# Kernel optimization log

Hardware: AMD Instinct MI355X
Metric: run time of the kernel (lower is better)

Reference implementation:

```python
import jax, jax.numpy as jnp
import numpy as np

H = 256  # hidden_dim
B = 256  # batch
T = 512  # seq_len


def setup_inputs() -> dict:
    key = jax.random.key(0)
    ks = jax.random.split(key, 16)
    s_in = 1.0  # torch LSTMCell init: U(-1/sqrt(H), 1/sqrt(H)); use scaled normal for simplicity
    sc = 1.0 / np.sqrt(H)
    inp = {
        "input": jax.random.normal(ks[0], (B, T), dtype=jnp.float32),
        # layer 1: input_size = 1
        "W_ih1": jax.random.uniform(ks[1], (4 * H, 1), jnp.float32, -sc, sc),
        "W_hh1": jax.random.uniform(ks[2], (4 * H, H), jnp.float32, -sc, sc),
        "b_ih1": jax.random.uniform(ks[3], (4 * H,), jnp.float32, -sc, sc),
        "b_hh1": jax.random.uniform(ks[4], (4 * H,), jnp.float32, -sc, sc),
        # layer 2
        "W_ih2": jax.random.uniform(ks[5], (4 * H, H), jnp.float32, -sc, sc),
        "W_hh2": jax.random.uniform(ks[6], (4 * H, H), jnp.float32, -sc, sc),
        "b_ih2": jax.random.uniform(ks[7], (4 * H,), jnp.float32, -sc, sc),
        "b_hh2": jax.random.uniform(ks[8], (4 * H,), jnp.float32, -sc, sc),
        # layer 3
        "W_ih3": jax.random.uniform(ks[9], (4 * H, H), jnp.float32, -sc, sc),
        "W_hh3": jax.random.uniform(ks[10], (4 * H, H), jnp.float32, -sc, sc),
        "b_ih3": jax.random.uniform(ks[11], (4 * H,), jnp.float32, -sc, sc),
        "b_hh3": jax.random.uniform(ks[12], (4 * H,), jnp.float32, -sc, sc),
        # output head Linear(H, 1)
        "W_lin": jax.random.uniform(ks[13], (1, H), jnp.float32, -sc, sc),
        "b_lin": jax.random.uniform(ks[14], (1,), jnp.float32, -sc, sc),
    }
    return inp


def _lstm_cell(x, h, c, Wi, Wh, bi, bh):
    # PyTorch LSTMCell gate order: i, f, g, o
    gates = x @ Wi.T + bi + h @ Wh.T + bh  # [B, 4H]
    i, f, g, o = jnp.split(gates, 4, axis=-1)
    c_new = jax.nn.sigmoid(f) * c + jax.nn.sigmoid(i) * jnp.tanh(g)
    h_new = jax.nn.sigmoid(o) * jnp.tanh(c_new)
    return h_new, c_new


def reference(input, W_ih1, W_hh1, b_ih1, b_hh1, W_ih2, W_hh2, b_ih2, b_hh2,
              W_ih3, W_hh3, b_ih3, b_hh3, W_lin, b_lin):
    n = input.shape[0]
    z = jnp.zeros((n, H), dtype=jnp.float32)
    init = (z, z, z, z, z, z)  # (h1, c1, h2, c2, h3, c3)
    xs = input.T[:, :, None]  # [T, B, 1]

    def step(carry, x_t):
        h1, c1, h2, c2, h3, c3 = carry
        h1, c1 = _lstm_cell(x_t, h1, c1, W_ih1, W_hh1, b_ih1, b_hh1)
        h2, c2 = _lstm_cell(h1, h2, c2, W_ih2, W_hh2, b_ih2, b_hh2)
        h3, c3 = _lstm_cell(h2, h3, c3, W_ih3, W_hh3, b_ih3, b_hh3)
        y = h3 @ W_lin.T + b_lin  # [B, 1] (dropout p=0 is identity)
        return (h1, c1, h2, c2, h3, c3), y

    _, ys = jax.lax.scan(step, init, xs)  # ys: [T, B, 1]
    return ys[:, :, 0].T  # [B, T], matches torch.cat(outputs, dim=1)
```

## Files before the change

kernel.cpp:

```cpp
#include <hip/hip_runtime.h>
#include <stdint.h>


#define Hd 256
#define Bd 256
#define Td 512
#define RING 4
#define GH 8
#define GB 8
#define CPAD 32

typedef __attribute__((ext_vector_type(8))) short short8;
typedef __attribute__((ext_vector_type(4))) float floatx4;
typedef __attribute__((ext_vector_type(4))) unsigned int uintx4;

__device__ __forceinline__ unsigned short f2bf(float f) {
  union { float f; unsigned int u; } v; v.f = f;
  return (unsigned short)((v.u + 0x7fffu + ((v.u >> 16) & 1u)) >> 16);
}
__device__ __forceinline__ float sigm(float x) { return 1.0f / (1.0f + __expf(-x)); }
__device__ __forceinline__ float tanhfast(float x) { return 2.0f / (1.0f + __expf(-2.0f * x)) - 1.0f; }

__device__ __forceinline__ void spin_relaxed(unsigned int* p, unsigned int v) {
  while (__hip_atomic_load(p, __ATOMIC_RELAXED, __HIP_MEMORY_SCOPE_AGENT) < v) { }
}

__global__ __launch_bounds__(512, 2) void lstm3_kernel(
    const float* __restrict__ xin,
    const float* __restrict__ Wi1, const float* __restrict__ Wh1,
    const float* __restrict__ bi1, const float* __restrict__ bh1,
    const float* __restrict__ Wi2, const float* __restrict__ Wh2,
    const float* __restrict__ bi2, const float* __restrict__ bh2,
    const float* __restrict__ Wi3, const float* __restrict__ Wh3,
    const float* __restrict__ bi3, const float* __restrict__ bh3,
    const float* __restrict__ Wlin, const float* __restrict__ blin,
    float* __restrict__ out,
    unsigned int* __restrict__ cnt,
    unsigned short* __restrict__ ring)
{
  __shared__ float gl[4][32][33];
  __shared__ uintx4 hbuf[2][1024];

  const int bid = blockIdx.x;
  const int j   = bid / 24;
  const int rem = bid - j * 24;
  const int l   = rem >> 3;
  const int g   = rem & 7;

  const int tid  = threadIdx.x;
  const int lane = tid & 63;
  const int wave = tid >> 6;
  const int tau  = wave & 3;
  const int mh   = wave >> 2;
  const int quad = lane >> 4;
  const int l15  = lane & 15;

  const int ubase = j * 32;
  const int rbase = g * 32;

  const float* Wpi = (l == 1) ? Wi2 : Wi3;
  const float* Wph = (l == 0) ? Wh1 : ((l == 1) ? Wh2 : Wh3);
  const float* bi  = (l == 0) ? bi1 : ((l == 1) ? bi2 : bi3);
  const float* bh  = (l == 0) ? bh1 : ((l == 1) ? bh2 : bh3);

  short8 breg[2][16];
  {
    const int koff = quad * 8;
    #pragma unroll
    for (int nt = 0; nt < 2; ++nt) {
      const int grow = tau * Hd + ubase + nt * 16 + l15;
      #pragma unroll
      for (int kc = 0; kc < 16; ++kc) {
        short8 v = {0, 0, 0, 0, 0, 0, 0, 0};
        const float* src = nullptr;
        if (kc < 8) { if (l != 0) src = Wpi + (size_t)grow * Hd + kc * 32 + koff; }
        else        { src = Wph + (size_t)grow * Hd + (kc - 8) * 32 + koff; }
        if (src) {
          #pragma unroll
          for (int e = 0; e < 8; ++e) v[e] = (short)f2bf(src[e]);
        }
        breg[nt][kc] = v;
      }
    }
  }

  const int clrow = tid >> 4;
  const int cu0   = (tid & 15) * 2;
  float bsum[4][2], wiv[4][2], wlv[2];
  #pragma unroll
  for (int tt = 0; tt < 4; ++tt) {
    #pragma unroll
    for (int du = 0; du < 2; ++du) {
      const int gg = tt * Hd + ubase + cu0 + du;
      bsum[tt][du] = bi[gg] + bh[gg];
      wiv[tt][du]  = (l == 0) ? Wi1[gg] : 0.0f;
    }
  }
  wlv[0] = (l == 2) ? Wlin[ubase + cu0]     : 0.0f;
  wlv[1] = (l == 2) ? Wlin[ubase + cu0 + 1] : 0.0f;
  const float bl0 = (l == 2 && j == 0) ? blin[0] : 0.0f;

  float cst0 = 0.0f, cst1 = 0.0f;

  unsigned int* myC = cnt + (l * GB + g) * CPAD;
  unsigned int* upC = cnt + ((l - 1) * GB + g) * CPAD;
  unsigned int* dnC = cnt + ((l + 1) * GB + g) * CPAD;
  unsigned short* ownR = ring + (size_t)l * RING * Bd * Hd;
  const unsigned short* upRb = ring + (size_t)(l - 1) * RING * Bd * Hd;

  const float* xrow = xin + (size_t)(rbase + clrow) * Td;

  const int c0 = tid;
  const int c1 = tid + 512;
  const int o0 = ((c0 >> 2) & 31) * 512 + (c0 >> 7) * 64 + (c0 & 3) * 16;
  const int o1 = ((c1 >> 2) & 31) * 512 + (c1 >> 7) * 64 + (c1 & 3) * 16;
  const int fragbase = (mh * 16 + l15) * 4 + quad;

  {
    uintx4 z = {0u, 0u, 0u, 0u};
    hbuf[1][c0] = z;
    hbuf[1][c1] = z;
  }

  for (int t = 0; t < Td; ++t) {
    {
      bool active = false; unsigned int* p = nullptr; unsigned need = 0;
      if (tid == 0)      { active = (t > 0);                p = myC; need = GH * t; }
      else if (tid == 1) { active = (l > 0);                p = upC; need = GH * (t + 1); }
      else if (tid == 2) { active = (l < 2) && (t >= RING); p = dnC; need = GH * (t - RING + 1); }
      if (active) spin_relaxed(p, need);
    }
    __syncthreads();

    uintx4 u0, u1, v0, v1;
    if (l != 0) {
      const char* upReg = (const char*)(upRb + (size_t)(t & (RING - 1)) * Bd * Hd
                                        + (size_t)rbase * Hd);
      asm volatile("global_load_dwordx4 %0, %1, off sc0 sc1"
                   : "=&v"(u0) : "v"(upReg + o0));
      asm volatile("global_load_dwordx4 %0, %1, off sc0 sc1"
                   : "=&v"(u1) : "v"(upReg + o1));
    }
    if (t != 0) {
      const char* ownReg = (const char*)(ownR + (size_t)((t + RING - 1) & (RING - 1)) * Bd * Hd
                                         + (size_t)rbase * Hd);
      asm volatile("global_load_dwordx4 %0, %1, off sc0 sc1"
                   : "=&v"(v0) : "v"(ownReg + o0));
      asm volatile("global_load_dwordx4 %0, %1, off sc0 sc1"
                   : "=&v"(v1) : "v"(ownReg + o1));
    }
    asm volatile("s_waitcnt vmcnt(0)" ::: "memory");
    if (l != 0) { hbuf[0][c0] = u0; hbuf[0][c1] = u1; }
    if (t != 0) { hbuf[1][c0] = v0; hbuf[1][c1] = v1; }
    __syncthreads();

    short8 av[16];
    if (l != 0) {
      #pragma unroll
      for (int kc = 0; kc < 8; ++kc)
        av[kc] = *reinterpret_cast<const short8*>(&hbuf[0][kc * 128 + fragbase]);
    }
    #pragma unroll
    for (int kc = 0; kc < 8; ++kc)
      av[8 + kc] = *reinterpret_cast<const short8*>(&hbuf[1][kc * 128 + fragbase]);

    floatx4 acc0 = {0.f, 0.f, 0.f, 0.f};
    floatx4 acc1 = {0.f, 0.f, 0.f, 0.f};
    if (l != 0) {
      #pragma unroll
      for (int kc = 0; kc < 8; ++kc) {
        acc0 = __builtin_amdgcn_mfma_f32_16x16x32_bf16(av[kc], breg[0][kc], acc0, 0, 0, 0);
        acc1 = __builtin_amdgcn_mfma_f32_16x16x32_bf16(av[kc], breg[1][kc], acc1, 0, 0, 0);
      }
    }
    #pragma unroll
    for (int kc = 8; kc < 16; ++kc) {
      acc0 = __builtin_amdgcn_mfma_f32_16x16x32_bf16(av[kc], breg[0][kc], acc0, 0, 0, 0);
      acc1 = __builtin_amdgcn_mfma_f32_16x16x32_bf16(av[kc], breg[1][kc], acc1, 0, 0, 0);
    }

    {
      const int lr = mh * 16 + quad * 4;
      #pragma unroll
      for (int r2 = 0; r2 < 4; ++r2) {
        gl[tau][lr + r2][l15]      = acc0[r2];
        gl[tau][lr + r2][16 + l15] = acc1[r2];
      }
    }
    __syncthreads();

    float h0, h1;
    {
      const float xv = (l == 0) ? xrow[t] : 0.0f;
      float pi = gl[0][clrow][cu0] + bsum[0][0] + xv * wiv[0][0];
      float pf = gl[1][clrow][cu0] + bsum[1][0] + xv * wiv[1][0];
      float pg = gl[2][clrow][cu0] + bsum[2][0] + xv * wiv[2][0];
      float po = gl[3][clrow][cu0] + bsum[3][0] + xv * wiv[3][0];
      float ii = sigm(pi), ff = sigm(pf), gv = tanhfast(pg), oo = sigm(po);
      cst0 = ff * cst0 + ii * gv;
      h0 = oo * tanhfast(cst0);
      pi = gl[0][clrow][cu0 + 1] + bsum[0][1] + xv * wiv[0][1];
      pf = gl[1][clrow][cu0 + 1] + bsum[1][1] + xv * wiv[1][1];
      pg = gl[2][clrow][cu0 + 1] + bsum[2][1] + xv * wiv[2][1];
      po = gl[3][clrow][cu0 + 1] + bsum[3][1] + xv * wiv[3][1];
      ii = sigm(pi); ff = sigm(pf); gv = tanhfast(pg); oo = sigm(po);
      cst1 = ff * cst1 + ii * gv;
      h1 = oo * tanhfast(cst1);
    }

    {
      unsigned short* dst = ownR + (size_t)(t & (RING - 1)) * Bd * Hd
                          + (size_t)(rbase + clrow) * Hd + ubase + cu0;
      const unsigned int packed = (unsigned int)f2bf(h0) | ((unsigned int)f2bf(h1) << 16);
      __hip_atomic_store((unsigned int*)dst, packed, __ATOMIC_RELAXED,
                         __HIP_MEMORY_SCOPE_AGENT);
    }

    if (l == 2) {
      float pr = wlv[0] * h0 + wlv[1] * h1;
      pr += __shfl_xor(pr, 8);
      pr += __shfl_xor(pr, 4);
      pr += __shfl_xor(pr, 2);
      pr += __shfl_xor(pr, 1);
      if ((tid & 15) == 0) {
        atomicAdd(&out[(size_t)(rbase + clrow) * Td + t], pr + bl0);
      }
    }

    __syncthreads();
    if (tid == 0) {
      __hip_atomic_fetch_add(myC, 1u, __ATOMIC_RELAXED, __HIP_MEMORY_SCOPE_AGENT);
    }
  }
}

extern "C" void kernel_launch(void* const* d_in, const int* in_sizes, int n_in,
                              void* d_out, int out_size, void* d_ws, size_t ws_size,
                              hipStream_t stream) {
  const float* xin  = (const float*)d_in[0];
  const float* Wi1  = (const float*)d_in[1];
  const float* Wh1  = (const float*)d_in[2];
  const float* bi1  = (const float*)d_in[3];
  const float* bh1  = (const float*)d_in[4];
  const float* Wi2  = (const float*)d_in[5];
  const float* Wh2  = (const float*)d_in[6];
  const float* bi2  = (const float*)d_in[7];
  const float* bh2  = (const float*)d_in[8];
  const float* Wi3  = (const float*)d_in[9];
  const float* Wh3  = (const float*)d_in[10];
  const float* bi3  = (const float*)d_in[11];
  const float* bh3  = (const float*)d_in[12];
  const float* Wlin = (const float*)d_in[13];
  const float* blin = (const float*)d_in[14];
  float* out = (float*)d_out;

  unsigned int*   cnt  = (unsigned int*)d_ws;
  unsigned short* ring = (unsigned short*)((char*)d_ws + 4096);

  hipMemsetAsync(d_ws, 0, 4096, stream);
  hipMemsetAsync(d_out, 0, (size_t)out_size * sizeof(float), stream);

  lstm3_kernel<<<dim3(3 * GB * GH), dim3(512), 0, stream>>>(
      xin, Wi1, Wh1, bi1, bh1, Wi2, Wh2, bi2, bh2,
      Wi3, Wh3, bi3, bh3, Wlin, blin, out, cnt, ring);
}
```

Measured before the change: 1.663 ms.

## Double threads per block to split gate columns across more waves

Raises the block size from 512 to 1024 threads so each wave computes one 16-column MFMA tile instead of two, halving per-wave weight registers and per-thread loads and cell updates. The h-state store now packs neighbouring units through a lane shuffle, and the output reduction covers 32 lanes. This shortens each thread's serial work per timestep, since the recurrence is latency bound, but allows only one block per CU and adds more waves to every barrier.

```diff
diff --git a/kernel.cpp b/kernel.cpp
--- a/kernel.cpp
+++ b/kernel.cpp
@@ -25,7 +25,7 @@
   while (__hip_atomic_load(p, __ATOMIC_RELAXED, __HIP_MEMORY_SCOPE_AGENT) < v) { }
 }
 
-__global__ __launch_bounds__(512, 2) void lstm3_kernel(
+__global__ __launch_bounds__(1024, 1) void lstm3_kernel(
     const float* __restrict__ xin,
     const float* __restrict__ Wi1, const float* __restrict__ Wh1,
     const float* __restrict__ bi1, const float* __restrict__ bh1,
@@ -51,7 +51,8 @@
   const int lane = tid & 63;
   const int wave = tid >> 6;
   const int tau  = wave & 3;
-  const int mh   = wave >> 2;
+  const int mh   = (wave >> 2) & 1;
+  const int ub   = wave >> 3;
   const int quad = lane >> 4;
   const int l15  = lane & 15;
 
@@ -63,44 +64,37 @@
   const float* bi  = (l == 0) ? bi1 : ((l == 1) ? bi2 : bi3);
   const float* bh  = (l == 0) ? bh1 : ((l == 1) ? bh2 : bh3);
 
-  short8 breg[2][16];
+  short8 breg[16];
   {
     const int koff = quad * 8;
+    const int grow = tau * Hd + ubase + ub * 16 + l15;
     #pragma unroll
-    for (int nt = 0; nt < 2; ++nt) {
-      const int grow = tau * Hd + ubase + nt * 16 + l15;
-      #pragma unroll
-      for (int kc = 0; kc < 16; ++kc) {
-        short8 v = {0, 0, 0, 0, 0, 0, 0, 0};
-        const float* src = nullptr;
-        if (kc < 8) { if (l != 0) src = Wpi + (size_t)grow * Hd + kc * 32 + koff; }
-        else        { src = Wph + (size_t)grow * Hd + (kc - 8) * 32 + koff; }
-        if (src) {
-          #pragma unroll
-          for (int e = 0; e < 8; ++e) v[e] = (short)f2bf(src[e]);
-        }
-        breg[nt][kc] = v;
-      }
-    }
-  }
-
-  const int clrow = tid >> 4;
-  const int cu0   = (tid & 15) * 2;
-  float bsum[4][2], wiv[4][2], wlv[2];
+    for (int kc = 0; kc < 16; ++kc) {
+      short8 v = {0, 0, 0, 0, 0, 0, 0, 0};
+      const float* src = nullptr;
+      if (kc < 8) { if (l != 0) src = Wpi + (size_t)grow * Hd + kc * 32 + koff; }
+      else        { src = Wph + (size_t)grow * Hd + (kc - 8) * 32 + koff; }
+      if (src) {
+        #pragma unroll
+        for (int e = 0; e < 8; ++e) v[e] = (short)f2bf(src[e]);
+      }
+      breg[kc] = v;
+    }
+  }
+
+  const int clrow = tid >> 5;
+  const int cu    = tid & 31;
+  float bsum[4], wiv[4];
   #pragma unroll
   for (int tt = 0; tt < 4; ++tt) {
-    #pragma unroll
-    for (int du = 0; du < 2; ++du) {
-      const int gg = tt * Hd + ubase + cu0 + du;
-      bsum[tt][du] = bi[gg] + bh[gg];
-      wiv[tt][du]  = (l == 0) ? Wi1[gg] : 0.0f;
-    }
-  }
-  wlv[0] = (l == 2) ? Wlin[ubase + cu0]     : 0.0f;
-  wlv[1] = (l == 2) ? Wlin[ubase + cu0 + 1] : 0.0f;
+    const int gg = tt * Hd + ubase + cu;
+    bsum[tt] = bi[gg] + bh[gg];
+    wiv[tt]  = (l == 0) ? Wi1[gg] : 0.0f;
+  }
+  const float wlv = (l == 2) ? Wlin[ubase + cu] : 0.0f;
   const float bl0 = (l == 2 && j == 0) ? blin[0] : 0.0f;
 
-  float cst0 = 0.0f, cst1 = 0.0f;
+  float cst = 0.0f;
 
   unsigned int* myC = cnt + (l * GB + g) * CPAD;
   unsigned int* upC = cnt + ((l - 1) * GB + g) * CPAD;
@@ -111,15 +105,12 @@
   const float* xrow = xin + (size_t)(rbase + clrow) * Td;
 
   const int c0 = tid;
-  const int c1 = tid + 512;
-  const int o0 = ((c0 >> 2) & 31) * 512 + (c0 >> 7) * 64 + (c0 & 3) * 16;
-  const int o1 = ((c1 >> 2) & 31) * 512 + (c1 >> 7) * 64 + (c1 & 3) * 16;
+  const int o0 = ((tid >> 2) & 31) * 512 + (tid >> 7) * 64 + (tid & 3) * 16;
   const int fragbase = (mh * 16 + l15) * 4 + quad;
 
   {
     uintx4 z = {0u, 0u, 0u, 0u};
     hbuf[1][c0] = z;
-    hbuf[1][c1] = z;
   }
 
   for (int t = 0; t < Td; ++t) {
@@ -132,97 +123,78 @@
     }
     __syncthreads();
 
-    uintx4 u0, u1, v0, v1;
+    uintx4 u0, v0;
     if (l != 0) {
       const char* upReg = (const char*)(upRb + (size_t)(t & (RING - 1)) * Bd * Hd
                                         + (size_t)rbase * Hd);
       asm volatile("global_load_dwordx4 %0, %1, off sc0 sc1"
                    : "=&v"(u0) : "v"(upReg + o0));
-      asm volatile("global_load_dwordx4 %0, %1, off sc0 sc1"
-                   : "=&v"(u1) : "v"(upReg + o1));
     }
     if (t != 0) {
       const char* ownReg = (const char*)(ownR + (size_t)((t + RING - 1) & (RING - 1)) * Bd * Hd
                                          + (size_t)rbase * Hd);
       asm volatile("global_load_dwordx4 %0, %1, off sc0 sc1"
                    : "=&v"(v0) : "v"(ownReg + o0));
-      asm volatile("global_load_dwordx4 %0, %1, off sc0 sc1"
-                   : "=&v"(v1) : "v"(ownReg + o1));
     }
     asm volatile("s_waitcnt vmcnt(0)" ::: "memory");
-    if (l != 0) { hbuf[0][c0] = u0; hbuf[0][c1] = u1; }
-    if (t != 0) { hbuf[1][c0] = v0; hbuf[1][c1] = v1; }
-    __syncthreads();
-
-    short8 av[16];
-    if (l != 0) {
-      #pragma unroll
-      for (int kc = 0; kc < 8; ++kc)
-        av[kc] = *reinterpret_cast<const short8*>(&hbuf[0][kc * 128 + fragbase]);
-    }
-    #pragma unroll
-    for (int kc = 0; kc < 8; ++kc)
-      av[8 + kc] = *reinterpret_cast<const short8*>(&hbuf[1][kc * 128 + fragbase]);
-
-    floatx4 acc0 = {0.f, 0.f, 0.f, 0.f};
-    floatx4 acc1 = {0.f, 0.f, 0.f, 0.f};
+    if (l != 0) { hbuf[0][c0] = u0; }
+    if (t != 0) { hbuf[1][c0] = v0; }
+    __syncthreads();
+
+    floatx4 acc = {0.f, 0.f, 0.f, 0.f};
     if (l != 0) {
       #pragma unroll
       for (int kc = 0; kc < 8; ++kc) {
-        acc0 = __builtin_amdgcn_mfma_f32_16x16x32_bf16(av[kc], breg[0][kc], acc0, 0, 0, 0);
-        acc1 = __builtin_amdgcn_mfma_f32_16x16x32_bf16(av[kc], breg[1][kc], acc1, 0, 0, 0);
+        const short8 av = *reinterpret_cast<const short8*>(&hbuf[0][kc * 128 + fragbase]);
+        acc = __builtin_amdgcn_mfma_f32_16x16x32_bf16(av, breg[kc], acc, 0, 0, 0);
       }
     }
     #pragma unroll
     for (int kc = 8; kc < 16; ++kc) {
-      acc0 = __builtin_amdgcn_mfma_f32_16x16x32_bf16(av[kc], breg[0][kc], acc0, 0, 0, 0);
-      acc1 = __builtin_amdgcn_mfma_f32_16x16x32_bf16(av[kc], breg[1][kc], acc1, 0, 0, 0);
+      const short8 av = *reinterpret_cast<const short8*>(&hbuf[1][(kc - 8) * 128 + fragbase]);
+      acc = __builtin_amdgcn_mfma_f32_16x16x32_bf16(av, breg[kc], acc, 0, 0, 0);
     }
 
     {
       const int lr = mh * 16 + quad * 4;
       #pragma unroll
       for (int r2 = 0; r2 < 4; ++r2) {
-        gl[tau][lr + r2][l15]      = acc0[r2];
-        gl[tau][lr + r2][16 + l15] = acc1[r2];
-      }
-    }
-    __syncthreads();
-
-    float h0, h1;
+        gl[tau][lr + r2][ub * 16 + l15] = acc[r2];
+      }
+    }
+    __syncthreads();
+
+    float h0;
     {
       const float xv = (l == 0) ? xrow[t] : 0.0f;
-      float pi = gl[0][clrow][cu0] + bsum[0][0] + xv * wiv[0][0];
-      float pf = gl[1][clrow][cu0] + bsum[1][0] + xv * wiv[1][0];
-      float pg = gl[2][clrow][cu0] + bsum[2][0] + xv * wiv[2][0];
-      float po = gl[3][clrow][cu0] + bsum[3][0] + xv * wiv[3][0];
-      float ii = sigm(pi), ff = sigm(pf), gv = tanhfast(pg), oo = sigm(po);
-      cst0 = ff * cst0 + ii * gv;
-      h0 = oo * tanhfast(cst0);
-      pi = gl[0][clrow][cu0 + 1] + bsum[0][1] + xv * wiv[0][1];
-      pf = gl[1][clrow][cu0 + 1] + bsum[1][1] + xv * wiv[1][1];
-      pg = gl[2][clrow][cu0 + 1] + bsum[2][1] + xv * wiv[2][1];
-      po = gl[3][clrow][cu0 + 1] + bsum[3][1] + xv * wiv[3][1];
-      ii = sigm(pi); ff = sigm(pf); gv = tanhfast(pg); oo = sigm(po);
-      cst1 = ff * cst1 + ii * gv;
-      h1 = oo * tanhfast(cst1);
-    }
-
-    {
-      unsigned short* dst = ownR + (size_t)(t & (RING - 1)) * Bd * Hd
-                          + (size_t)(rbase + clrow) * Hd + ubase + cu0;
-      const unsigned int packed = (unsigned int)f2bf(h0) | ((unsigned int)f2bf(h1) << 16);
-      __hip_atomic_store((unsigned int*)dst, packed, __ATOMIC_RELAXED,
-                         __HIP_MEMORY_SCOPE_AGENT);
+      const float pi = gl[0][clrow][cu] + bsum[0] + xv * wiv[0];
+      const float pf = gl[1][clrow][cu] + bsum[1] + xv * wiv[1];
+      const float pg = gl[2][clrow][cu] + bsum[2] + xv * wiv[2];
+      const float po = gl[3][clrow][cu] + bsum[3] + xv * wiv[3];
+      const float ii = sigm(pi), ff = sigm(pf), gv = tanhfast(pg), oo = sigm(po);
+      cst = ff * cst + ii * gv;
+      h0 = oo * tanhfast(cst);
+    }
+
+    {
+      const float hn = __shfl_xor(h0, 1);
+      if ((cu & 1) == 0) {
+        unsigned short* dst = ownR + (size_t)(t & (RING - 1)) * Bd * Hd
+                            + (size_t)(rbase + clrow) * Hd + ubase + cu;
+        const unsigned int packed = (unsigned int)f2bf(h0) | ((unsigned int)f2bf(hn) << 16);
+        __hip_atomic_store((unsigned int*)dst, packed, __ATOMIC_RELAXED,
+                           __HIP_MEMORY_SCOPE_AGENT);
+      }
     }
 
     if (l == 2) {
-      float pr = wlv[0] * h0 + wlv[1] * h1;
+      float pr = wlv * h0;
+      pr += __shfl_xor(pr, 16);
       pr += __shfl_xor(pr, 8);
       pr += __shfl_xor(pr, 4);
       pr += __shfl_xor(pr, 2);
       pr += __shfl_xor(pr, 1);
-      if ((tid & 15) == 0) {
+      if ((tid & 31) == 0) {
         atomicAdd(&out[(size_t)(rbase + clrow) * Td + t], pr + bl0);
       }
     }
@@ -260,7 +232,7 @@
   hipMemsetAsync(d_ws, 0, 4096, stream);
   hipMemsetAsync(d_out, 0, (size_t)out_size * sizeof(float), stream);
 
-  lstm3_kernel<<<dim3(3 * GB * GH), dim3(512), 0, stream>>>(
+  lstm3_kernel<<<dim3(3 * GB * GH), dim3(1024), 0, stream>>>(
       xin, Wi1, Wh1, bi1, bh1, Wi2, Wh2, bi2, bh2,
       Wi3, Wh3, bi3, bh3, Wlin, blin, out, cnt, ring);
 }
```

Result: slower. 1.880 ms (+13.0%).
